# Kernel tuning notes

Hardware: AMD Instinct MI355X
Metric: run time of the kernel (lower is better)

Reference implementation:

```python
import jax, jax.numpy as jnp
import numpy as np

N_NODES = 100000
N_EDGES = 1600000
N_FEAT = 128
HIDDEN = 64
N_CLASSES = 40


def _gcn_layer(x, W, b, src, dst, w, n):
    # Linear transform first (as in torch_geometric GCNConv), then normalized aggregation.
    h = x @ W  # [N, out]
    # Add self-loops with weight 1.
    loop = jnp.arange(n, dtype=src.dtype)
    src_f = jnp.concatenate([src, loop])
    dst_f = jnp.concatenate([dst, loop])
    w_f = jnp.concatenate([w, jnp.ones((n,), dtype=w.dtype)])
    # Symmetric normalization deg^-1/2 * w * deg^-1/2 (deg computed at dst).
    deg = jax.ops.segment_sum(w_f, dst_f, num_segments=n)
    dinv = jnp.where(deg > 0, jax.lax.rsqrt(deg), 0.0)
    norm = dinv[src_f] * w_f * dinv[dst_f]  # [E+N]
    # Gather-scale-scatter aggregation.
    out = jax.ops.segment_sum(norm[:, None] * h[src_f], dst_f, num_segments=n)
    return out + b


def setup_inputs() -> dict:
    key = jax.random.key(0)
    ks = jax.random.split(key, 7)
    x = jax.random.normal(ks[0], (N_NODES, N_FEAT), dtype=jnp.float32)
    edge_index = jax.random.randint(ks[1], (2, N_EDGES), 0, N_NODES, dtype=jnp.int64)
    edge_weight = jax.random.uniform(ks[2], (N_EDGES,), dtype=jnp.float32)
    # Glorot-ish init for the two GCNConv linear weights.
    W1 = jax.random.normal(ks[3], (N_FEAT, HIDDEN), dtype=jnp.float32) * (1.0 / np.sqrt(N_FEAT))
    b1 = jnp.zeros((HIDDEN,), dtype=jnp.float32)
    W2 = jax.random.normal(ks[4], (HIDDEN, N_CLASSES), dtype=jnp.float32) * (1.0 / np.sqrt(HIDDEN))
    b2 = jnp.zeros((N_CLASSES,), dtype=jnp.float32)
    return {"x": x, "edge_index": edge_index, "edge_weight": edge_weight,
            "W1": W1, "b1": b1, "W2": W2, "b2": b2}


def reference(x, edge_index, edge_weight, W1, b1, W2, b2):
    n = x.shape[0]
    src, dst = edge_index[0], edge_index[1]
    h = jax.nn.relu(_gcn_layer(x, W1, b1, src, dst, edge_weight, n))
    # F.dropout(training=self.training): inference mode -> identity.
    h = _gcn_layer(h, W2, b2, src, dst, edge_weight, n)
    return jax.nn.log_softmax(h, axis=1)
```

## Files before the change

### kernel.cpp

```cpp
#include <hip/hip_runtime.h>
#include <hip/hip_bf16.h>
#include <math.h>


#define NFEAT 128
#define HID 64
#define NCLS 40
#define PB 512
#define BSH 7
#define NBUK_MAX 1024

static __device__ __forceinline__ unsigned short f2bf(float f) {
    unsigned u = __float_as_uint(f);
    unsigned r = (u + 0x7fffu + ((u >> 16) & 1u)) >> 16;
    return (unsigned short)r;
}
static __device__ __forceinline__ float bf2f(unsigned short b) {
    return __uint_as_float(((unsigned)b) << 16);
}

__global__ __launch_bounds__(256) void k_hist(const int* __restrict__ dst,
                                              int* __restrict__ ghist,
                                              int e, int nbuk, int epb) {
    __shared__ int hist[NBUK_MAX];
    for (int j = threadIdx.x; j < nbuk; j += 256) hist[j] = 0;
    __syncthreads();
    int b = blockIdx.x;
    int lo = b * epb, hi = min(lo + epb, e);
    for (int i = lo + threadIdx.x; i < hi; i += 256)
        atomicAdd(&hist[dst[i] >> BSH], 1);
    __syncthreads();
    for (int j = threadIdx.x; j < nbuk; j += 256) ghist[j * PB + b] = hist[j];
}

__global__ __launch_bounds__(256) void k_colscan(int* __restrict__ ghist,
                                                 int* __restrict__ buktot, int nbuk) {
    __shared__ int s[256];
    int k = blockIdx.x, t = threadIdx.x;
    int* col = ghist + k * PB;
    int v0 = col[2 * t], v1 = col[2 * t + 1];
    int sum = v0 + v1;
    s[t] = sum; __syncthreads();
    for (int off = 1; off < 256; off <<= 1) {
        int x = (t >= off) ? s[t - off] : 0;
        __syncthreads();
        s[t] += x;
        __syncthreads();
    }
    int excl = s[t] - sum;
    col[2 * t] = excl;
    col[2 * t + 1] = excl + v0;
    if (t == 255) buktot[k] = s[255];
}

__global__ __launch_bounds__(256) void k_bukscan(const int* __restrict__ buktot,
                                                 int* __restrict__ bukstart,
                                                 int* __restrict__ rowptr,
                                                 int nbuk, int n, int e) {
    __shared__ int s[256];
    int t = threadIdx.x;
    int v[4]; int sum = 0;
#pragma unroll
    for (int j = 0; j < 4; j++) { int idx = t * 4 + j; v[j] = (idx < nbuk) ? buktot[idx] : 0; sum += v[j]; }
    s[t] = sum; __syncthreads();
    for (int off = 1; off < 256; off <<= 1) {
        int x = (t >= off) ? s[t - off] : 0;
        __syncthreads();
        s[t] += x;
        __syncthreads();
    }
    int excl = s[t] - sum;
#pragma unroll
    for (int j = 0; j < 4; j++) { int idx = t * 4 + j; if (idx < nbuk) bukstart[idx] = excl; excl += v[j]; }
    if (t == 255) bukstart[nbuk] = s[255];
    if (t == 0) rowptr[n] = e;
}

__global__ __launch_bounds__(256) void k_bucketize(const int* __restrict__ src,
                                                   const int* __restrict__ dst,
                                                   const float* __restrict__ w,
                                                   const int* __restrict__ ghist,
                                                   const int* __restrict__ bukstart,
                                                   unsigned long long* __restrict__ sedge,
                                                   int e, int nbuk, int epb) {
    __shared__ int loff[NBUK_MAX];
    int b = blockIdx.x;
    for (int j = threadIdx.x; j < nbuk; j += 256) loff[j] = bukstart[j] + ghist[j * PB + b];
    __syncthreads();
    int lo = b * epb, hi = min(lo + epb, e);
    for (int i = lo + threadIdx.x; i < hi; i += 256) {
        int d = dst[i], s = src[i];
        int k = d >> BSH;
        int pos = atomicAdd(&loff[k], 1);
        unsigned long long rec = ((unsigned long long)__float_as_uint(w[i]) << 32)
                               | ((unsigned)(d & 127) << 17) | (unsigned)s;
        sedge[pos] = rec;
    }
}

__global__ __launch_bounds__(256) void k_bucket_csr(const unsigned long long* __restrict__ sedge,
                                                    const int* __restrict__ bukstart,
                                                    int* __restrict__ rowptr,
                                                    float* __restrict__ dinv,
                                                    int2* __restrict__ edges, int n) {
    __shared__ int cnt[128]; __shared__ float wsum[128];
    __shared__ int fill[128]; __shared__ int rloc[128];
    int k = blockIdx.x, t = threadIdx.x;
    int base = k << BSH;
    int nloc = n - base; if (nloc > 128) nloc = 128;
    if (t < 128) { cnt[t] = 0; fill[t] = 0; wsum[t] = 1.0f; }
    __syncthreads();
    int lo = bukstart[k], hi = bukstart[k + 1];
    for (int p = lo + t; p < hi; p += 256) {
        unsigned long long r = sedge[p];
        int dloc = (int)((r >> 17) & 127);
        atomicAdd(&cnt[dloc], 1);
        atomicAdd(&wsum[dloc], __uint_as_float((unsigned)(r >> 32)));
    }
    __syncthreads();
    if (t < 128) rloc[t] = cnt[t];
    __syncthreads();
    for (int off = 1; off < 128; off <<= 1) {
        int x = 0;
        if (t < 128 && t >= off) x = rloc[t - off];
        __syncthreads();
        if (t < 128) rloc[t] += x;
        __syncthreads();
    }
    if (t < 128) {
        int excl = rloc[t] - cnt[t];
        rloc[t] = excl;
        if (t < nloc) {
            rowptr[base + t] = lo + excl;
            dinv[base + t] = rsqrtf(wsum[t]);
        }
    }
    __syncthreads();
    for (int p = lo + t; p < hi; p += 256) {
        unsigned long long r = sedge[p];
        int dloc = (int)((r >> 17) & 127);
        int srcn = (int)(r & 0x1ffff);
        int pos = lo + rloc[dloc] + atomicAdd(&fill[dloc], 1);
        edges[pos] = make_int2((dloc << 17) | srcn, (int)(unsigned)(r >> 32));
    }
}

__global__ __launch_bounds__(256) void k_norm(const int* __restrict__ bukstart,
                                              const float* __restrict__ dinv,
                                              int2* __restrict__ edges, int n) {
    int k = blockIdx.x;
    int base = k << BSH;
    int lo = bukstart[k], hi = bukstart[k + 1];
    for (int p = lo + threadIdx.x; p < hi; p += 256) {
        int2 rec = edges[p];
        int dloc = rec.x >> 17, srcn = rec.x & 0x1ffff;
        float v = __int_as_float(rec.y) * dinv[srcn] * dinv[base + dloc];
        edges[p] = make_int2(srcn, __float_as_int(v));
    }
}

__global__ __launch_bounds__(256) void k_gemm1(const float* __restrict__ x,
                                               const float* __restrict__ W1,
                                               unsigned short* __restrict__ h1, int n) {
    __shared__ float xs[64 * 65];
    int t = threadIdx.x;
    int lane = t & 63;
    int wid = __builtin_amdgcn_readfirstlane(t >> 6);
    int base = blockIdx.x * 64;
    int nrows = n - base; if (nrows > 64) nrows = 64;
    const float4* xg = reinterpret_cast<const float4*>(x + (size_t)base * NFEAT);
    float acc[16];
#pragma unroll
    for (int c = 0; c < 16; c++) acc[c] = 0.f;
#pragma unroll
    for (int h = 0; h < 2; h++) {
        for (int j = t; j < nrows * 16; j += 256) {
            int row = j >> 4, k4 = j & 15;
            float4 v = xg[row * 32 + h * 16 + k4];
            xs[(4 * k4 + 0) * 65 + row] = v.x;
            xs[(4 * k4 + 1) * 65 + row] = v.y;
            xs[(4 * k4 + 2) * 65 + row] = v.z;
            xs[(4 * k4 + 3) * 65 + row] = v.w;
        }
        __syncthreads();
        const float* wb = W1 + (size_t)(h * 64) * HID + wid * 16;
#pragma unroll 4
        for (int k = 0; k < 64; k++) {
            float xv = xs[k * 65 + lane];
            const float* wk = wb + k * HID;
#pragma unroll
            for (int c = 0; c < 16; c++) acc[c] = fmaf(wk[c], xv, acc[c]);
        }
        __syncthreads();
    }
    if (lane < nrows) {
        unsigned pk[8];
#pragma unroll
        for (int j = 0; j < 8; j++)
            pk[j] = (unsigned)f2bf(acc[2 * j]) | ((unsigned)f2bf(acc[2 * j + 1]) << 16);
        uint4* hp = reinterpret_cast<uint4*>(h1 + (size_t)(base + lane) * HID + wid * 16);
        hp[0] = make_uint4(pk[0], pk[1], pk[2], pk[3]);
        hp[1] = make_uint4(pk[4], pk[5], pk[6], pk[7]);
    }
}

__global__ __launch_bounds__(256) void k_agg1(const unsigned short* __restrict__ h1,
                                              const int* __restrict__ rowptr,
                                              const int2* __restrict__ edges,
                                              const float* __restrict__ dinv,
                                              const float* __restrict__ b1,
                                              unsigned short* __restrict__ y, int n) {
    int lane = threadIdx.x & 63;
    int wid = threadIdx.x >> 6;
    for (int node = blockIdx.x * 4 + wid; node < n; node += gridDim.x * 4) {
        int i = __builtin_amdgcn_readfirstlane(node);
        float di = dinv[i];
        float a0 = di * di * bf2f(h1[(size_t)i * HID + lane]);
        float a1 = 0.f, a2 = 0.f, a3 = 0.f, a4 = 0.f, a5 = 0.f, a6 = 0.f, a7 = 0.f;
        int s = rowptr[i], e = rowptr[i + 1];
        int p = s;
        for (; p + 8 <= e; p += 8) {
            int2 e0 = edges[p], e1 = edges[p + 1], e2 = edges[p + 2], e3 = edges[p + 3];
            int2 e4 = edges[p + 4], e5 = edges[p + 5], e6 = edges[p + 6], e7 = edges[p + 7];
            a0 = fmaf(__int_as_float(e0.y), bf2f(h1[(size_t)e0.x * HID + lane]), a0);
            a1 = fmaf(__int_as_float(e1.y), bf2f(h1[(size_t)e1.x * HID + lane]), a1);
            a2 = fmaf(__int_as_float(e2.y), bf2f(h1[(size_t)e2.x * HID + lane]), a2);
            a3 = fmaf(__int_as_float(e3.y), bf2f(h1[(size_t)e3.x * HID + lane]), a3);
            a4 = fmaf(__int_as_float(e4.y), bf2f(h1[(size_t)e4.x * HID + lane]), a4);
            a5 = fmaf(__int_as_float(e5.y), bf2f(h1[(size_t)e5.x * HID + lane]), a5);
            a6 = fmaf(__int_as_float(e6.y), bf2f(h1[(size_t)e6.x * HID + lane]), a6);
            a7 = fmaf(__int_as_float(e7.y), bf2f(h1[(size_t)e7.x * HID + lane]), a7);
        }
        for (; p + 4 <= e; p += 4) {
            int2 e0 = edges[p], e1 = edges[p + 1], e2 = edges[p + 2], e3 = edges[p + 3];
            a0 = fmaf(__int_as_float(e0.y), bf2f(h1[(size_t)e0.x * HID + lane]), a0);
            a1 = fmaf(__int_as_float(e1.y), bf2f(h1[(size_t)e1.x * HID + lane]), a1);
            a2 = fmaf(__int_as_float(e2.y), bf2f(h1[(size_t)e2.x * HID + lane]), a2);
            a3 = fmaf(__int_as_float(e3.y), bf2f(h1[(size_t)e3.x * HID + lane]), a3);
        }
        for (; p < e; p++) {
            int2 e0 = edges[p];
            a0 = fmaf(__int_as_float(e0.y), bf2f(h1[(size_t)e0.x * HID + lane]), a0);
        }
        float acc = ((a0 + a1) + (a2 + a3)) + ((a4 + a5) + (a6 + a7)) + b1[lane];
        y[(size_t)i * HID + lane] = f2bf(fmaxf(acc, 0.f));
    }
}

__global__ __launch_bounds__(256) void k_aggz(const unsigned short* __restrict__ y,
                                              const int* __restrict__ rowptr,
                                              const int2* __restrict__ edges,
                                              const float* __restrict__ dinv,
                                              float* __restrict__ z, int n) {
    int lane = threadIdx.x & 63;
    int wid = threadIdx.x >> 6;
    for (int node = blockIdx.x * 4 + wid; node < n; node += gridDim.x * 4) {
        int i = __builtin_amdgcn_readfirstlane(node);
        float di = dinv[i];
        float a0 = di * di * bf2f(y[(size_t)i * HID + lane]);
        float a1 = 0.f, a2 = 0.f, a3 = 0.f, a4 = 0.f, a5 = 0.f, a6 = 0.f, a7 = 0.f;
        int s = rowptr[i], e = rowptr[i + 1];
        int p = s;
        for (; p + 8 <= e; p += 8) {
            int2 e0 = edges[p], e1 = edges[p + 1], e2 = edges[p + 2], e3 = edges[p + 3];
            int2 e4 = edges[p + 4], e5 = edges[p + 5], e6 = edges[p + 6], e7 = edges[p + 7];
            a0 = fmaf(__int_as_float(e0.y), bf2f(y[(size_t)e0.x * HID + lane]), a0);
            a1 = fmaf(__int_as_float(e1.y), bf2f(y[(size_t)e1.x * HID + lane]), a1);
            a2 = fmaf(__int_as_float(e2.y), bf2f(y[(size_t)e2.x * HID + lane]), a2);
            a3 = fmaf(__int_as_float(e3.y), bf2f(y[(size_t)e3.x * HID + lane]), a3);
            a4 = fmaf(__int_as_float(e4.y), bf2f(y[(size_t)e4.x * HID + lane]), a4);
            a5 = fmaf(__int_as_float(e5.y), bf2f(y[(size_t)e5.x * HID + lane]), a5);
            a6 = fmaf(__int_as_float(e6.y), bf2f(y[(size_t)e6.x * HID + lane]), a6);
            a7 = fmaf(__int_as_float(e7.y), bf2f(y[(size_t)e7.x * HID + lane]), a7);
        }
        for (; p + 4 <= e; p += 4) {
            int2 e0 = edges[p], e1 = edges[p + 1], e2 = edges[p + 2], e3 = edges[p + 3];
            a0 = fmaf(__int_as_float(e0.y), bf2f(y[(size_t)e0.x * HID + lane]), a0);
            a1 = fmaf(__int_as_float(e1.y), bf2f(y[(size_t)e1.x * HID + lane]), a1);
            a2 = fmaf(__int_as_float(e2.y), bf2f(y[(size_t)e2.x * HID + lane]), a2);
            a3 = fmaf(__int_as_float(e3.y), bf2f(y[(size_t)e3.x * HID + lane]), a3);
        }
        for (; p < e; p++) {
            int2 e0 = edges[p];
            a0 = fmaf(__int_as_float(e0.y), bf2f(y[(size_t)e0.x * HID + lane]), a0);
        }
        float acc = ((a0 + a1) + (a2 + a3)) + ((a4 + a5) + (a6 + a7));
        z[(size_t)i * HID + lane] = acc;
    }
}

__global__ __launch_bounds__(256) void k_gemm2s(const float* __restrict__ z,
                                                const float* __restrict__ W2,
                                                const float* __restrict__ b2,
                                                float* __restrict__ out, int n) {
    __shared__ float ys[HID * 65];
    __shared__ float zs[64 * 41];
    int t = threadIdx.x;
    int lane = t & 63;
    int wid = __builtin_amdgcn_readfirstlane(t >> 6);
    int base = blockIdx.x * 64;
    int nrows = n - base; if (nrows > 64) nrows = 64;
    const float4* yg = reinterpret_cast<const float4*>(z + (size_t)base * HID);
    for (int j = t; j < nrows * 16; j += 256) {
        int row = j >> 4, k4 = j & 15;
        float4 v = yg[j];
        ys[(4 * k4 + 0) * 65 + row] = v.x;
        ys[(4 * k4 + 1) * 65 + row] = v.y;
        ys[(4 * k4 + 2) * 65 + row] = v.z;
        ys[(4 * k4 + 3) * 65 + row] = v.w;
    }
    __syncthreads();
    const float* wb = W2 + wid * 10;
    float acc[10];
#pragma unroll
    for (int c = 0; c < 10; c++) acc[c] = b2[wid * 10 + c];
#pragma unroll 4
    for (int k = 0; k < HID; k++) {
        float yv = ys[k * 65 + lane];
        const float* wk = wb + k * NCLS;
#pragma unroll
        for (int c = 0; c < 10; c++) acc[c] = fmaf(wk[c], yv, acc[c]);
    }
#pragma unroll
    for (int c = 0; c < 10; c++) zs[lane * 41 + wid * 10 + c] = acc[c];
    __syncthreads();
    if (lane < nrows) {
        const float* zr = zs + lane * 41;
        float m = zr[0];
#pragma unroll
        for (int j = 1; j < NCLS; j++) m = fmaxf(m, zr[j]);
        float sum = 0.f;
#pragma unroll
        for (int j = 0; j < NCLS; j++) sum += expf(zr[j] - m);
        float lse = m + logf(sum);
        float2* op = reinterpret_cast<float2*>(out + (size_t)(base + lane) * NCLS + wid * 10);
#pragma unroll
        for (int j = 0; j < 5; j++)
            op[j] = make_float2(acc[2 * j] - lse, acc[2 * j + 1] - lse);
    }
}


extern "C" void kernel_launch(void* const* d_in, const int* in_sizes, int n_in,
                              void* d_out, int out_size, void* d_ws, size_t ws_size,
                              hipStream_t stream) {
    const float* x = (const float*)d_in[0];
    const int* edge_index = (const int*)d_in[1];
    const float* ew = (const float*)d_in[2];
    const float* W1 = (const float*)d_in[3];
    const float* b1 = (const float*)d_in[4];
    const float* W2 = (const float*)d_in[5];
    const float* b2 = (const float*)d_in[6];
    float* out = (float*)d_out;

    const int N = in_sizes[0] / NFEAT;
    const int E = in_sizes[2];
    const int* src = edge_index;
    const int* dst = edge_index + E;

    const int NBUK = (N + 127) >> BSH;
    const int EPB = (E + PB - 1) / PB;

    char* ws = (char*)d_ws;
    size_t off = 0;
    auto alloc = [&](size_t bytes) { void* p = ws + off; off = (off + bytes + 255) & ~(size_t)255; return p; };
    int*   ghist    = (int*)alloc((size_t)NBUK_MAX * PB * 4);
    int*   buktot   = (int*)alloc(4096);
    int*   bukstart = (int*)alloc(4096 + 4);
    int*   rowptr   = (int*)alloc((size_t)(N + 1) * 4);
    float* dinv     = (float*)alloc((size_t)N * 4);
    int2*  edges    = (int2*)alloc((size_t)E * 8);
    unsigned short* ybuf = (unsigned short*)alloc((size_t)N * HID * 2);
    void* uni = alloc((size_t)N * HID * 4);
    unsigned long long* sedge = (unsigned long long*)uni;
    unsigned short* h1 = (unsigned short*)uni;
    float* z = (float*)uni;

    k_hist<<<PB, 256, 0, stream>>>(dst, ghist, E, NBUK, EPB);
    k_colscan<<<NBUK, 256, 0, stream>>>(ghist, buktot, NBUK);
    k_bukscan<<<1, 256, 0, stream>>>(buktot, bukstart, rowptr, NBUK, N, E);
    k_bucketize<<<PB, 256, 0, stream>>>(src, dst, ew, ghist, bukstart, sedge, E, NBUK, EPB);
    k_bucket_csr<<<NBUK, 256, 0, stream>>>(sedge, bukstart, rowptr, dinv, edges, N);
    k_norm<<<NBUK, 256, 0, stream>>>(bukstart, dinv, edges, N);
    k_gemm1<<<(N + 63) / 64, 256, 0, stream>>>(x, W1, h1, N);
    k_agg1<<<(N + 3) / 4, 256, 0, stream>>>(h1, rowptr, edges, dinv, b1, ybuf, N);
    k_aggz<<<(N + 3) / 4, 256, 0, stream>>>(ybuf, rowptr, edges, dinv, z, N);
    k_gemm2s<<<(N + 63) / 64, 256, 0, stream>>>(z, W2, b2, out, N);
}
```

Before: 314.0 us.

## Split wavefront into 8 edge groups with 16-byte row loads in aggregation

Both aggregation kernels now split each wavefront into 8 groups of 8 lanes. Each group handles a different edge, and each lane loads 8 bf16 features with one 16-byte load instead of one 2-byte element per lane per edge. Partial sums are combined across groups with xor-shuffles, and only the first group writes the row using vector stores. This aims to cut the number of memory instructions and widen gather transactions, and adds cross-lane reduction work plus lane waste on low-degree nodes.

```diff
diff --git a/kernel.cpp b/kernel.cpp
--- a/kernel.cpp
+++ b/kernel.cpp
@@ -17,6 +17,12 @@
 }
 static __device__ __forceinline__ float bf2f(unsigned short b) {
     return __uint_as_float(((unsigned)b) << 16);
+}
+static __device__ __forceinline__ float bflo(unsigned u) {
+    return __uint_as_float(u << 16);
+}
+static __device__ __forceinline__ float bfhi(unsigned u) {
+    return __uint_as_float(u & 0xffff0000u);
 }
 
 __global__ __launch_bounds__(256) void k_hist(const int* __restrict__ dst,
@@ -204,6 +210,16 @@
     }
 }
 
+#define FMA8(acc, v, r)                                   \
+    acc[0] = fmaf(v, bflo(r.x), acc[0]);                  \
+    acc[1] = fmaf(v, bfhi(r.x), acc[1]);                  \
+    acc[2] = fmaf(v, bflo(r.y), acc[2]);                  \
+    acc[3] = fmaf(v, bfhi(r.y), acc[3]);                  \
+    acc[4] = fmaf(v, bflo(r.z), acc[4]);                  \
+    acc[5] = fmaf(v, bfhi(r.z), acc[5]);                  \
+    acc[6] = fmaf(v, bflo(r.w), acc[6]);                  \
+    acc[7] = fmaf(v, bfhi(r.w), acc[7]);
+
 __global__ __launch_bounds__(256) void k_agg1(const unsigned short* __restrict__ h1,
                                               const int* __restrict__ rowptr,
                                               const int2* __restrict__ edges,
@@ -212,38 +228,58 @@
                                               unsigned short* __restrict__ y, int n) {
     int lane = threadIdx.x & 63;
     int wid = threadIdx.x >> 6;
+    int g = lane >> 3;
+    int sl = lane & 7;
+    const float4* bp = reinterpret_cast<const float4*>(b1 + sl * 8);
+    float4 bA = bp[0], bB = bp[1];
+    float bcol[8] = {bA.x, bA.y, bA.z, bA.w, bB.x, bB.y, bB.z, bB.w};
+
     for (int node = blockIdx.x * 4 + wid; node < n; node += gridDim.x * 4) {
         int i = __builtin_amdgcn_readfirstlane(node);
         float di = dinv[i];
-        float a0 = di * di * bf2f(h1[(size_t)i * HID + lane]);
-        float a1 = 0.f, a2 = 0.f, a3 = 0.f, a4 = 0.f, a5 = 0.f, a6 = 0.f, a7 = 0.f;
+        float acc[8];
+#pragma unroll
+        for (int j = 0; j < 8; j++) acc[j] = 0.f;
+        if (g == 0) {
+            uint4 r = *reinterpret_cast<const uint4*>(h1 + (size_t)i * HID + sl * 8);
+            float s2 = di * di;
+            FMA8(acc, s2, r);
+        }
         int s = rowptr[i], e = rowptr[i + 1];
         int p = s;
-        for (; p + 8 <= e; p += 8) {
-            int2 e0 = edges[p], e1 = edges[p + 1], e2 = edges[p + 2], e3 = edges[p + 3];
-            int2 e4 = edges[p + 4], e5 = edges[p + 5], e6 = edges[p + 6], e7 = edges[p + 7];
-            a0 = fmaf(__int_as_float(e0.y), bf2f(h1[(size_t)e0.x * HID + lane]), a0);
-            a1 = fmaf(__int_as_float(e1.y), bf2f(h1[(size_t)e1.x * HID + lane]), a1);
-            a2 = fmaf(__int_as_float(e2.y), bf2f(h1[(size_t)e2.x * HID + lane]), a2);
-            a3 = fmaf(__int_as_float(e3.y), bf2f(h1[(size_t)e3.x * HID + lane]), a3);
-            a4 = fmaf(__int_as_float(e4.y), bf2f(h1[(size_t)e4.x * HID + lane]), a4);
-            a5 = fmaf(__int_as_float(e5.y), bf2f(h1[(size_t)e5.x * HID + lane]), a5);
-            a6 = fmaf(__int_as_float(e6.y), bf2f(h1[(size_t)e6.x * HID + lane]), a6);
-            a7 = fmaf(__int_as_float(e7.y), bf2f(h1[(size_t)e7.x * HID + lane]), a7);
-        }
-        for (; p + 4 <= e; p += 4) {
-            int2 e0 = edges[p], e1 = edges[p + 1], e2 = edges[p + 2], e3 = edges[p + 3];
-            a0 = fmaf(__int_as_float(e0.y), bf2f(h1[(size_t)e0.x * HID + lane]), a0);
-            a1 = fmaf(__int_as_float(e1.y), bf2f(h1[(size_t)e1.x * HID + lane]), a1);
-            a2 = fmaf(__int_as_float(e2.y), bf2f(h1[(size_t)e2.x * HID + lane]), a2);
-            a3 = fmaf(__int_as_float(e3.y), bf2f(h1[(size_t)e3.x * HID + lane]), a3);
-        }
-        for (; p < e; p++) {
-            int2 e0 = edges[p];
-            a0 = fmaf(__int_as_float(e0.y), bf2f(h1[(size_t)e0.x * HID + lane]), a0);
-        }
-        float acc = ((a0 + a1) + (a2 + a3)) + ((a4 + a5) + (a6 + a7)) + b1[lane];
-        y[(size_t)i * HID + lane] = f2bf(fmaxf(acc, 0.f));
+        for (; p + 16 <= e; p += 16) {
+            int2 erA = edges[p + g];
+            int2 erB = edges[p + 8 + g];
+            uint4 ra = *reinterpret_cast<const uint4*>(h1 + (size_t)erA.x * HID + sl * 8);
+            uint4 rb = *reinterpret_cast<const uint4*>(h1 + (size_t)erB.x * HID + sl * 8);
+            float va = __int_as_float(erA.y);
+            float vb = __int_as_float(erB.y);
+            FMA8(acc, va, ra);
+            FMA8(acc, vb, rb);
+        }
+        for (; p < e; p += 8) {
+            int pe = p + g;
+            int2 er = (pe < e) ? edges[pe] : make_int2(i, 0);
+            uint4 r = *reinterpret_cast<const uint4*>(h1 + (size_t)er.x * HID + sl * 8);
+            float v = __int_as_float(er.y);
+            FMA8(acc, v, r);
+        }
+#pragma unroll
+        for (int off = 8; off <= 32; off <<= 1) {
+#pragma unroll
+            for (int j = 0; j < 8; j++) acc[j] += __shfl_xor(acc[j], off);
+        }
+        if (g == 0) {
+            unsigned pk[4];
+#pragma unroll
+            for (int j = 0; j < 4; j++) {
+                float f0 = fmaxf(acc[2 * j] + bcol[2 * j], 0.f);
+                float f1 = fmaxf(acc[2 * j + 1] + bcol[2 * j + 1], 0.f);
+                pk[j] = (unsigned)f2bf(f0) | ((unsigned)f2bf(f1) << 16);
+            }
+            *reinterpret_cast<uint4*>(y + (size_t)i * HID + sl * 8) =
+                make_uint4(pk[0], pk[1], pk[2], pk[3]);
+        }
     }
 }
 
@@ -254,38 +290,48 @@
                                               float* __restrict__ z, int n) {
     int lane = threadIdx.x & 63;
     int wid = threadIdx.x >> 6;
+    int g = lane >> 3;
+    int sl = lane & 7;
     for (int node = blockIdx.x * 4 + wid; node < n; node += gridDim.x * 4) {
         int i = __builtin_amdgcn_readfirstlane(node);
         float di = dinv[i];
-        float a0 = di * di * bf2f(y[(size_t)i * HID + lane]);
-        float a1 = 0.f, a2 = 0.f, a3 = 0.f, a4 = 0.f, a5 = 0.f, a6 = 0.f, a7 = 0.f;
+        float acc[8];
+#pragma unroll
+        for (int j = 0; j < 8; j++) acc[j] = 0.f;
+        if (g == 0) {
+            uint4 r = *reinterpret_cast<const uint4*>(y + (size_t)i * HID + sl * 8);
+            float s2 = di * di;
+            FMA8(acc, s2, r);
+        }
         int s = rowptr[i], e = rowptr[i + 1];
         int p = s;
-        for (; p + 8 <= e; p += 8) {
-            int2 e0 = edges[p], e1 = edges[p + 1], e2 = edges[p + 2], e3 = edges[p + 3];
-            int2 e4 = edges[p + 4], e5 = edges[p + 5], e6 = edges[p + 6], e7 = edges[p + 7];
-            a0 = fmaf(__int_as_float(e0.y), bf2f(y[(size_t)e0.x * HID + lane]), a0);
-            a1 = fmaf(__int_as_float(e1.y), bf2f(y[(size_t)e1.x * HID + lane]), a1);
-            a2 = fmaf(__int_as_float(e2.y), bf2f(y[(size_t)e2.x * HID + lane]), a2);
-            a3 = fmaf(__int_as_float(e3.y), bf2f(y[(size_t)e3.x * HID + lane]), a3);
-            a4 = fmaf(__int_as_float(e4.y), bf2f(y[(size_t)e4.x * HID + lane]), a4);
-            a5 = fmaf(__int_as_float(e5.y), bf2f(y[(size_t)e5.x * HID + lane]), a5);
-            a6 = fmaf(__int_as_float(e6.y), bf2f(y[(size_t)e6.x * HID + lane]), a6);
-            a7 = fmaf(__int_as_float(e7.y), bf2f(y[(size_t)e7.x * HID + lane]), a7);
-        }
-        for (; p + 4 <= e; p += 4) {
-            int2 e0 = edges[p], e1 = edges[p + 1], e2 = edges[p + 2], e3 = edges[p + 3];
-            a0 = fmaf(__int_as_float(e0.y), bf2f(y[(size_t)e0.x * HID + lane]), a0);
-            a1 = fmaf(__int_as_float(e1.y), bf2f(y[(size_t)e1.x * HID + lane]), a1);
-            a2 = fmaf(__int_as_float(e2.y), bf2f(y[(size_t)e2.x * HID + lane]), a2);
-            a3 = fmaf(__int_as_float(e3.y), bf2f(y[(size_t)e3.x * HID + lane]), a3);
-        }
-        for (; p < e; p++) {
-            int2 e0 = edges[p];
-            a0 = fmaf(__int_as_float(e0.y), bf2f(y[(size_t)e0.x * HID + lane]), a0);
-        }
-        float acc = ((a0 + a1) + (a2 + a3)) + ((a4 + a5) + (a6 + a7));
-        z[(size_t)i * HID + lane] = acc;
+        for (; p + 16 <= e; p += 16) {
+            int2 erA = edges[p + g];
+            int2 erB = edges[p + 8 + g];
+            uint4 ra = *reinterpret_cast<const uint4*>(y + (size_t)erA.x * HID + sl * 8);
+            uint4 rb = *reinterpret_cast<const uint4*>(y + (size_t)erB.x * HID + sl * 8);
+            float va = __int_as_float(erA.y);
+            float vb = __int_as_float(erB.y);
+            FMA8(acc, va, ra);
+            FMA8(acc, vb, rb);
+        }
+        for (; p < e; p += 8) {
+            int pe = p + g;
+            int2 er = (pe < e) ? edges[pe] : make_int2(i, 0);
+            uint4 r = *reinterpret_cast<const uint4*>(y + (size_t)er.x * HID + sl * 8);
+            float v = __int_as_float(er.y);
+            FMA8(acc, v, r);
+        }
+#pragma unroll
+        for (int off = 8; off <= 32; off <<= 1) {
+#pragma unroll
+            for (int j = 0; j < 8; j++) acc[j] += __shfl_xor(acc[j], off);
+        }
+        if (g == 0) {
+            float* zp = z + (size_t)i * HID + sl * 8;
+            *reinterpret_cast<float4*>(zp) = make_float4(acc[0], acc[1], acc[2], acc[3]);
+            *reinterpret_cast<float4*>(zp + 4) = make_float4(acc[4], acc[5], acc[6], acc[7]);
+        }
     }
 }
 
```

New measurement: 305.2 us. 2.8% less time.
